# Optimization experiments

Measured on AMD Instinct MI355X. Metric: run time of the kernel, lower is better.

The kernel has to match this reference:

```python
import jax, jax.numpy as jnp
import numpy as np

N = 50000      # nodes
E = 500000     # directed edges
F_IN = 112     # node feature dim
G = 256        # number of graphs in batch


def _lin(key, fan_in, fan_out):
    # torch nn.Linear default init: U(-1/sqrt(fan_in), 1/sqrt(fan_in))
    s = 1.0 / np.sqrt(fan_in)
    kw, kb = jax.random.split(key)
    W = jax.random.uniform(kw, (fan_in, fan_out), jnp.float32, -s, s)
    b = jax.random.uniform(kb, (fan_out,), jnp.float32, -s, s)
    return W, b


def setup_inputs() -> dict:
    key = jax.random.key(0)
    ks = jax.random.split(key, 9)
    x = jax.random.normal(ks[0], (N, F_IN), jnp.float32)
    edge_index = jax.random.randint(ks[1], (2, E), 0, N)
    # sorted graph ids, guaranteeing every graph id 0..G-1 appears
    batch = jnp.sort(jnp.concatenate([jnp.arange(G),
                                      jax.random.randint(ks[2], (N - G,), 0, G)]))
    W1, b1 = _lin(ks[3], F_IN, 336)
    W2, b2 = _lin(ks[4], 336, 168)
    Wg, bg = _lin(ks[5], 168, 84)
    Wf, bf = _lin(ks[6], 84, 42)
    Wo, bo = _lin(ks[7], 42, 1)
    return dict(x=x, edge_index=edge_index, batch=batch,
                W1=W1, b1=b1, W2=W2, b2=b2,
                Wg=Wg, bg=bg, Wf=Wf, bf=bf, Wo=Wo, bo=bo)


def _gcn_conv(x, W, b, src, dst, n):
    """PyG GCNConv: add self-loops, symmetric D^-1/2 A D^-1/2 normalization."""
    h = x @ W                                   # [n, out]
    loop = jnp.arange(n, dtype=src.dtype)
    src_f = jnp.concatenate([src, loop])        # [E+n]
    dst_f = jnp.concatenate([dst, loop])
    deg = jax.ops.segment_sum(jnp.ones(src_f.shape[0], jnp.float32), dst_f, n)
    dinv = jnp.where(deg > 0, jax.lax.rsqrt(deg), 0.0)
    norm = dinv[src_f] * dinv[dst_f]            # [E+n]
    out = jax.ops.segment_sum(h[src_f] * norm[:, None], dst_f, n)
    return out + b


def reference(x, edge_index, batch, W1, b1, W2, b2, Wg, bg, Wf, bf, Wo, bo):
    src, dst = edge_index[0], edge_index[1]
    h = jax.nn.relu(_gcn_conv(x, W1, b1, src, dst, N))
    # dropout is identity in eval mode
    h = jax.nn.relu(_gcn_conv(h, W2, b2, src, dst, N))
    g = jax.ops.segment_max(h, batch, G)        # global max pool -> [G, 168]
    g = jax.nn.relu(g @ Wg + bg)
    g = jax.nn.relu(g @ Wf + bf)
    return g @ Wo + bo                           # [G, 1]
```

## Files before the change

### kernel.cpp

```cpp
#include <hip/hip_runtime.h>
#include <hip/hip_fp16.h>

#define N_NODES 50000
#define MPAD    50048
#define N_EDGES 500000
#define F_IN    112
#define K1P     128
#define F1      336
#define K2P     352
#define F2      168
#define NGRAPH  256
#define SCAN_CHUNK 1024
#define SCAN_BLOCKS ((N_NODES + SCAN_CHUNK - 1) / SCAN_CHUNK)

typedef __attribute__((ext_vector_type(8))) _Float16 f16x8;
typedef __attribute__((ext_vector_type(4))) float f32x4;
typedef unsigned short ushort_t;

__device__ __forceinline__ ushort_t f16_bits(float x) {
    __half h = __float2half_rn(x);
    return *(ushort_t*)&h;
}

__global__ void k_zero_int(int* p, int n) {
    int i = blockIdx.x * blockDim.x + threadIdx.x;
    if (i < n) p[i] = 0;
}

#define CVX_BLOCKS  ((N_NODES * 32) / 256)
#define CNT_BLOCKS  ((N_EDGES / 2 + 255) / 256)
#define CVW1_BLOCKS ((384 * K1P + 255) / 256)
#define CVW2_BLOCKS ((192 * K2P + 255) / 256)
#define RNG_BLOCKS  ((N_NODES + 255) / 256)
#define PREP_BLOCKS (CVX_BLOCKS + CNT_BLOCKS + CVW1_BLOCKS + CVW2_BLOCKS + RNG_BLOCKS)

__global__ __launch_bounds__(256) void k_prep(const float* __restrict__ x,
                                              const int* __restrict__ dst,
                                              const float* __restrict__ W1,
                                              const float* __restrict__ W2,
                                              const int* __restrict__ batch,
                                              ushort_t* __restrict__ x16,
                                              int* __restrict__ dcount,
                                              ushort_t* __restrict__ w1t,
                                              ushort_t* __restrict__ w2t,
                                              int* __restrict__ r0, int* __restrict__ r1) {
    int bid = blockIdx.x;
    int t = threadIdx.x;
    if (bid < CVX_BLOCKS) {
        int i = bid * 256 + t;
        int v = i >> 5, c = i & 31;
        uint2 u = {0, 0};
        if (c < 28) {
            float4 f = *(const float4*)&x[(long)v * F_IN + c * 4];
            __half2 h0 = __floats2half2_rn(f.x, f.y);
            __half2 h1 = __floats2half2_rn(f.z, f.w);
            u.x = *(unsigned*)&h0; u.y = *(unsigned*)&h1;
        }
        ((uint2*)x16)[i] = u;
        return;
    }
    bid -= CVX_BLOCKS;
    if (bid < CNT_BLOCKS) {
        int i = bid * 256 + t;
        if (i < N_EDGES / 2) {
            int2 d = ((const int2*)dst)[i];
            atomicAdd(&dcount[d.x], 1);
            atomicAdd(&dcount[d.y], 1);
        }
        return;
    }
    bid -= CNT_BLOCKS;
    if (bid < CVW1_BLOCKS) {
        int idx = bid * 256 + t;
        if (idx < 384 * K1P) {
            int n = idx / K1P, k = idx % K1P;
            float v = (n < F1 && k < F_IN) ? W1[k * F1 + n] : 0.0f;
            w1t[idx] = f16_bits(v);
        }
        return;
    }
    bid -= CVW1_BLOCKS;
    if (bid < CVW2_BLOCKS) {
        int idx = bid * 256 + t;
        if (idx < 192 * K2P) {
            int n = idx / K2P, k = idx % K2P;
            float v = (n < F2 && k < F1) ? W2[k * F2 + n] : 0.0f;
            w2t[idx] = f16_bits(v);
        }
        return;
    }
    bid -= CVW2_BLOCKS;
    {
        int v = bid * 256 + t;
        if (v >= N_NODES) return;
        int b = batch[v];
        if (v == 0 || batch[v - 1] != b) r0[b] = v;
        if (v == N_NODES - 1 || batch[v + 1] != b) r1[b] = v + 1;
    }
}

__global__ __launch_bounds__(SCAN_CHUNK) void k_scan1(const int* __restrict__ dcount,
                                                      int* __restrict__ off,
                                                      int* __restrict__ partials,
                                                      float* __restrict__ dinv, int n) {
    __shared__ int s[SCAN_CHUNK];
    int t = threadIdx.x;
    int i = blockIdx.x * SCAN_CHUNK + t;
    int val = (i < n) ? dcount[i] : 0;
    s[t] = val;
    __syncthreads();
    for (int d = 1; d < SCAN_CHUNK; d <<= 1) {
        int x = (t >= d) ? s[t - d] : 0;
        __syncthreads();
        s[t] += x;
        __syncthreads();
    }
    if (i < n) {
        off[i] = s[t] - val;
        dinv[i] = rsqrtf((float)val + 1.0f);
    }
    if (t == SCAN_CHUNK - 1) partials[blockIdx.x] = s[t];
}
__global__ __launch_bounds__(SCAN_CHUNK) void k_scan3(int* __restrict__ off,
                                                      const int* __restrict__ partials, int n) {
    __shared__ int tmp[SCAN_BLOCKS];
    __shared__ int pref[SCAN_BLOCKS];
    int t = threadIdx.x;
    if (t < SCAN_BLOCKS) tmp[t] = partials[t];
    __syncthreads();
    if (t == 0) {
        int run = 0;
        for (int j = 0; j < SCAN_BLOCKS; ++j) { pref[j] = run; run += tmp[j]; }
    }
    __syncthreads();
    int i = blockIdx.x * SCAN_CHUNK + t;
    if (i < n) off[i] += pref[blockIdx.x];
    if (i == n) off[i] = N_EDGES;
}

__global__ void k_scatter(const int* __restrict__ src, const int* __restrict__ dst,
                          const int* __restrict__ off, int* __restrict__ cur,
                          const float* __restrict__ dinv,
                          int2* __restrict__ csr, int e2) {
    int i = blockIdx.x * blockDim.x + threadIdx.x;
    if (i >= e2) return;
    int2 s2 = ((const int2*)src)[i];
    int2 d2 = ((const int2*)dst)[i];
    {
        int pos = atomicAdd(&cur[d2.x], 1);
        int2 rec; rec.x = s2.x; rec.y = __float_as_int(dinv[s2.x] * dinv[d2.x]);
        csr[off[d2.x] + pos] = rec;
    }
    {
        int pos = atomicAdd(&cur[d2.y], 1);
        int2 rec; rec.x = s2.y; rec.y = __float_as_int(dinv[s2.y] * dinv[d2.y]);
        csr[off[d2.y] + pos] = rec;
    }
}

__global__ __launch_bounds__(256) void k_agg1(const ushort_t* __restrict__ X16,
                                              const int* __restrict__ off,
                                              const int2* __restrict__ csr,
                                              const float* __restrict__ dinv,
                                              ushort_t* __restrict__ aX) {
    int w = (blockIdx.x * 256 + threadIdx.x) >> 6;
    int lane = threadIdx.x & 63;
    if (w >= N_NODES / 2) return;
    const int g = lane >> 5, sl = lane & 31;
    const int v = 2 * w + g;
    int o0A = off[2 * w], oM = off[2 * w + 1], o1B = off[2 * w + 2];
    int o0 = g ? oM : o0A;
    int n  = g ? (o1B - oM) : (oM - o0A);
    int nmax = max(oM - o0A, o1B - oM);
    float di = dinv[v];
    float s2 = di * di;
    uint2 us = *(const uint2*)(X16 + (long)v * K1P + sl * 4);
    float2 sf0 = __half22float2(*(__half2*)&us.x);
    float2 sf1 = __half22float2(*(__half2*)&us.y);
    float4 acc = {sf0.x * s2, sf0.y * s2, sf1.x * s2, sf1.y * s2};
    int nm1 = max(n - 1, 0);
    for (int b = 0; b < nmax; b += 8) {
        int2 e[8];
        #pragma unroll
        for (int j = 0; j < 8; ++j) {
            int cidx = min(o0 + min(b + j, nm1), N_EDGES - 1);
            e[j] = csr[cidx];
        }
        uint2 u[8];
        #pragma unroll
        for (int j = 0; j < 8; ++j)
            u[j] = *(const uint2*)(X16 + (long)e[j].x * K1P + sl * 4);
        #pragma unroll
        for (int j = 0; j < 8; ++j) {
            float c = ((b + j) < n) ? __int_as_float(e[j].y) : 0.0f;
            float2 f0 = __half22float2(*(__half2*)&u[j].x);
            float2 f1 = __half22float2(*(__half2*)&u[j].y);
            acc.x += c * f0.x; acc.y += c * f0.y; acc.z += c * f1.x; acc.w += c * f1.y;
        }
    }
    __half2 h0 = __floats2half2_rn(acc.x, acc.y);
    __half2 h1 = __floats2half2_rn(acc.z, acc.w);
    uint2 o; o.x = *(unsigned*)&h0; o.y = *(unsigned*)&h1;
    *(uint2*)(aX + (long)v * K1P + sl * 4) = o;
}

__global__ __launch_bounds__(256) void k_gemm_fused(
        const ushort_t* __restrict__ aX,
        const ushort_t* __restrict__ w1t,
        const float* __restrict__ b1,
        const ushort_t* __restrict__ w2t,
        ushort_t* __restrict__ T2) {
    __shared__ ushort_t As[64][40];
    __shared__ ushort_t Bs[352][40];
    __shared__ ushort_t H1s[64][360];
    const int tid = threadIdx.x;
    const int row0 = blockIdx.x * 64;
    const int w = tid >> 6, l = tid & 63;
    const int wm = w >> 1, wn = w & 1;
    const int lm = l & 15, lq = l >> 4;

    f32x4 acc1[2][11];
    #pragma unroll
    for (int i = 0; i < 2; ++i)
        #pragma unroll
        for (int j = 0; j < 11; ++j) acc1[i][j] = (f32x4){0.f, 0.f, 0.f, 0.f};

    for (int k0 = 0; k0 < K1P; k0 += 32) {
        {
            int r = tid >> 2, s = (tid & 3) * 8;
            *(int4*)&As[r][s] = *(const int4*)&aX[(long)(row0 + r) * K1P + k0 + s];
        }
        #pragma unroll
        for (int it = 0; it < 6; ++it) {
            int f = tid + it * 256;
            if (f < 1408) {
                int r = f >> 2, s = (f & 3) * 8;
                *(int4*)&Bs[r][s] = *(const int4*)&w1t[(long)r * K1P + k0 + s];
            }
        }
        __syncthreads();
        f16x8 af0 = *(const f16x8*)&As[wm * 32 + lm][lq * 8];
        f16x8 af1 = *(const f16x8*)&As[wm * 32 + 16 + lm][lq * 8];
        #pragma unroll
        for (int ns = 0; ns < 11; ++ns) {
            f16x8 bf = *(const f16x8*)&Bs[wn * 176 + ns * 16 + lm][lq * 8];
            acc1[0][ns] = __builtin_amdgcn_mfma_f32_16x16x32_f16(af0, bf, acc1[0][ns], 0, 0, 0);
            acc1[1][ns] = __builtin_amdgcn_mfma_f32_16x16x32_f16(af1, bf, acc1[1][ns], 0, 0, 0);
        }
        __syncthreads();
    }
    #pragma unroll
    for (int ms = 0; ms < 2; ++ms)
        #pragma unroll
        for (int ns = 0; ns < 11; ++ns) {
            int col = wn * 176 + ns * 16 + lm;
            float bb = (col < F1) ? b1[col] : 0.0f;
            #pragma unroll
            for (int i = 0; i < 4; ++i) {
                int r = wm * 32 + ms * 16 + lq * 4 + i;
                H1s[r][col] = f16_bits(fmaxf(acc1[ms][ns][i] + bb, 0.0f));
            }
        }
    __syncthreads();

    f32x4 acc2[2][6];
    #pragma unroll
    for (int i = 0; i < 2; ++i)
        #pragma unroll
        for (int j = 0; j < 6; ++j) acc2[i][j] = (f32x4){0.f, 0.f, 0.f, 0.f};

    for (int k0 = 0; k0 < K2P; k0 += 32) {
        #pragma unroll
        for (int it = 0; it < 3; ++it) {
            int f = tid + it * 256;
            int r = f >> 2, s = (f & 3) * 8;
            *(int4*)&Bs[r][s] = *(const int4*)&w2t[(long)r * K2P + k0 + s];
        }
        __syncthreads();
        f16x8 af0 = *(const f16x8*)&H1s[wm * 32 + lm][k0 + lq * 8];
        f16x8 af1 = *(const f16x8*)&H1s[wm * 32 + 16 + lm][k0 + lq * 8];
        #pragma unroll
        for (int ns = 0; ns < 6; ++ns) {
            f16x8 bf = *(const f16x8*)&Bs[wn * 96 + ns * 16 + lm][lq * 8];
            acc2[0][ns] = __builtin_amdgcn_mfma_f32_16x16x32_f16(af0, bf, acc2[0][ns], 0, 0, 0);
            acc2[1][ns] = __builtin_amdgcn_mfma_f32_16x16x32_f16(af1, bf, acc2[1][ns], 0, 0, 0);
        }
        __syncthreads();
    }
    #pragma unroll
    for (int ms = 0; ms < 2; ++ms)
        #pragma unroll
        for (int ns = 0; ns < 6; ++ns) {
            int col = wn * 96 + ns * 16 + lm;
            if (col < F2) {
                #pragma unroll
                for (int i = 0; i < 4; ++i) {
                    int r = row0 + wm * 32 + ms * 16 + lq * 4 + i;
                    T2[(long)r * F2 + col] = f16_bits(acc2[ms][ns][i]);
                }
            }
        }
}

__global__ __launch_bounds__(256) void k_agg2(const ushort_t* __restrict__ T16,
                                              const int* __restrict__ off,
                                              const int2* __restrict__ csr,
                                              const float* __restrict__ dinv,
                                              const float* __restrict__ b2,
                                              ushort_t* __restrict__ out2) {
    int w = (blockIdx.x * 256 + threadIdx.x) >> 6;
    int lane = threadIdx.x & 63;
    if (w >= N_NODES / 2) return;
    const int g = lane >> 5, sl = lane & 31;
    const int v = 2 * w + g;
    const bool act = sl < 21;
    int o0A = off[2 * w], oM = off[2 * w + 1], o1B = off[2 * w + 2];
    int o0 = g ? oM : o0A;
    int n  = g ? (o1B - oM) : (oM - o0A);
    int nmax = max(oM - o0A, o1B - oM);
    float di = dinv[v];
    float4 a0 = {0, 0, 0, 0}, a1 = {0, 0, 0, 0};
    if (act) {
        uint4 u = *(const uint4*)(T16 + (long)v * F2 + sl * 8);
        float2 f0 = __half22float2(*(__half2*)&u.x);
        float2 f1 = __half22float2(*(__half2*)&u.y);
        float2 f2 = __half22float2(*(__half2*)&u.z);
        float2 f3 = __half22float2(*(__half2*)&u.w);
        float s2 = di * di;
        a0.x = f0.x * s2; a0.y = f0.y * s2; a0.z = f1.x * s2; a0.w = f1.y * s2;
        a1.x = f2.x * s2; a1.y = f2.y * s2; a1.z = f3.x * s2; a1.w = f3.y * s2;
    }
    int nm1 = max(n - 1, 0);
    for (int b = 0; b < nmax; b += 8) {
        int2 e[8];
        #pragma unroll
        for (int j = 0; j < 8; ++j) {
            int cidx = min(o0 + min(b + j, nm1), N_EDGES - 1);
            e[j] = csr[cidx];
        }
        uint4 u[8];
        #pragma unroll
        for (int j = 0; j < 8; ++j) {
            int s = ((b + j) < n) ? e[j].x : v;
            if (act) u[j] = *(const uint4*)(T16 + (long)s * F2 + sl * 8);
        }
        #pragma unroll
        for (int j = 0; j < 8; ++j) {
            float c = ((b + j) < n) ? __int_as_float(e[j].y) : 0.0f;
            float2 f0 = __half22float2(*(__half2*)&u[j].x);
            float2 f1 = __half22float2(*(__half2*)&u[j].y);
            float2 f2 = __half22float2(*(__half2*)&u[j].z);
            float2 f3 = __half22float2(*(__half2*)&u[j].w);
            a0.x += c * f0.x; a0.y += c * f0.y; a0.z += c * f1.x; a0.w += c * f1.y;
            a1.x += c * f2.x; a1.y += c * f2.y; a1.z += c * f3.x; a1.w += c * f3.y;
        }
    }
    if (act) {
        float4 bb0 = ((const float4*)b2)[sl * 2];
        float4 bb1 = ((const float4*)b2)[sl * 2 + 1];
        __half2 h0 = __floats2half2_rn(fmaxf(a0.x + bb0.x, 0.0f), fmaxf(a0.y + bb0.y, 0.0f));
        __half2 h1 = __floats2half2_rn(fmaxf(a0.z + bb0.z, 0.0f), fmaxf(a0.w + bb0.w, 0.0f));
        __half2 h2 = __floats2half2_rn(fmaxf(a1.x + bb1.x, 0.0f), fmaxf(a1.y + bb1.y, 0.0f));
        __half2 h3 = __floats2half2_rn(fmaxf(a1.z + bb1.z, 0.0f), fmaxf(a1.w + bb1.w, 0.0f));
        uint4 o;
        o.x = *(unsigned*)&h0; o.y = *(unsigned*)&h1;
        o.z = *(unsigned*)&h2; o.w = *(unsigned*)&h3;
        *(uint4*)(out2 + (long)v * F2 + sl * 8) = o;
    }
}

__global__ __launch_bounds__(256) void k_pool_head(const ushort_t* __restrict__ out2,
        const int* __restrict__ r0, const int* __restrict__ r1,
        const float* __restrict__ Wg, const float* __restrict__ bg,
        const float* __restrict__ Wf, const float* __restrict__ bf,
        const float* __restrict__ Wo, const float* __restrict__ bo,
        float* __restrict__ out) {
    __shared__ float4 sm[4][F2 / 4];
    __shared__ float s0[F2];
    __shared__ float s1[84];
    __shared__ float s2[42];
    int gi = blockIdx.x;
    int slot = threadIdx.x >> 6, lane = threadIdx.x & 63;
    int a = r0[gi], b = r1[gi];
    if (lane < F2 / 4) {
        float4 mx = {0, 0, 0, 0};
        for (int v = a + slot; v < b; v += 4) {
            uint2 u = ((const uint2*)(out2 + (long)v * F2))[lane];
            float2 f0 = __half22float2(*(__half2*)&u.x);
            float2 f1 = __half22float2(*(__half2*)&u.y);
            mx.x = fmaxf(mx.x, f0.x); mx.y = fmaxf(mx.y, f0.y);
            mx.z = fmaxf(mx.z, f1.x); mx.w = fmaxf(mx.w, f1.y);
        }
        sm[slot][lane] = mx;
    }
    __syncthreads();
    if (slot == 0 && lane < F2 / 4) {
        float4 m0 = sm[0][lane], m1 = sm[1][lane], m2 = sm[2][lane], m3 = sm[3][lane];
        float4 r;
        r.x = fmaxf(fmaxf(m0.x, m1.x), fmaxf(m2.x, m3.x));
        r.y = fmaxf(fmaxf(m0.y, m1.y), fmaxf(m2.y, m3.y));
        r.z = fmaxf(fmaxf(m0.z, m1.z), fmaxf(m2.z, m3.z));
        r.w = fmaxf(fmaxf(m0.w, m1.w), fmaxf(m2.w, m3.w));
        ((float4*)s0)[lane] = r;
    }
    __syncthreads();
    int t = threadIdx.x;
    if (t < 84) {
        float acc = bg[t];
        #pragma unroll 4
        for (int k = 0; k < F2; ++k) acc += s0[k] * Wg[k * 84 + t];
        s1[t] = fmaxf(acc, 0.0f);
    }
    __syncthreads();
    if (t < 42) {
        float acc = bf[t];
        #pragma unroll 4
        for (int k = 0; k < 84; ++k) acc += s1[k] * Wf[k * 42 + t];
        s2[t] = fmaxf(acc, 0.0f);
    }
    __syncthreads();
    if (t == 0) {
        float acc = bo[0];
        for (int k = 0; k < 42; ++k) acc += s2[k] * Wo[k];
        out[gi] = acc;
    }
}

extern "C" void kernel_launch(void* const* d_in, const int* in_sizes, int n_in,
                              void* d_out, int out_size, void* d_ws, size_t ws_size,
                              hipStream_t stream) {
    const float* x   = (const float*)d_in[0];
    const int*   ei  = (const int*)d_in[1];
    const int*   bat = (const int*)d_in[2];
    const float* W1  = (const float*)d_in[3];
    const float* b1  = (const float*)d_in[4];
    const float* W2  = (const float*)d_in[5];
    const float* b2  = (const float*)d_in[6];
    const float* Wg  = (const float*)d_in[7];
    const float* bg  = (const float*)d_in[8];
    const float* Wf  = (const float*)d_in[9];
    const float* bf  = (const float*)d_in[10];
    const float* Wo  = (const float*)d_in[11];
    const float* bo  = (const float*)d_in[12];
    float* out = (float*)d_out;

    char* p = (char*)d_ws;
    float* dinv     = (float*)p; p += 50048 * 4;
    int*   dcount   = (int*)p;   p += 50048 * 4;
    int*   cur      = (int*)p;   p += 50048 * 4;
    int*   off      = (int*)p;   p += 50064 * 4;
    int*   partials = (int*)p;   p += 64 * 4;
    int*   rng0     = (int*)p;   p += 256 * 4;
    int*   rng1     = (int*)p;   p += 256 * 4;
    int2*  csr      = (int2*)p;  p += (long)N_EDGES * 8;
    ushort_t* x16   = (ushort_t*)p; p += (long)N_NODES * K1P * 2;
    ushort_t* aX    = (ushort_t*)p; p += (long)MPAD * K1P * 2;
    ushort_t* w1t   = (ushort_t*)p; p += (long)384 * K1P * 2;
    ushort_t* w2t   = (ushort_t*)p; p += (long)192 * K2P * 2;
    ushort_t* t16   = (ushort_t*)p; p += (long)MPAD * F2 * 2;
    ushort_t* o16   = (ushort_t*)p; p += (long)N_NODES * F2 * 2;

    const int* src = ei;
    const int* dst = ei + N_EDGES;
    const int B = 256;

    k_zero_int<<<(2 * 50048 + B - 1) / B, B, 0, stream>>>(dcount, 2 * 50048);
    k_prep<<<PREP_BLOCKS, B, 0, stream>>>(x, dst, W1, W2, bat, x16, dcount, w1t, w2t, rng0, rng1);
    k_scan1<<<SCAN_BLOCKS, SCAN_CHUNK, 0, stream>>>(dcount, off, partials, dinv, N_NODES);
    k_scan3<<<SCAN_BLOCKS, SCAN_CHUNK, 0, stream>>>(off, partials, N_NODES);
    k_scatter<<<(N_EDGES / 2 + B - 1) / B, B, 0, stream>>>(src, dst, off, cur, dinv, csr, N_EDGES / 2);

    k_agg1<<<(N_NODES / 2 * 64) / 256, 256, 0, stream>>>(x16, off, csr, dinv, aX);
    k_gemm_fused<<<MPAD / 64, 256, 0, stream>>>(aX, w1t, b1, w2t, t16);

    k_agg2<<<(N_NODES / 2 * 64) / 256, 256, 0, stream>>>(t16, off, csr, dinv, b2, o16);

    k_pool_head<<<NGRAPH, 256, 0, stream>>>(o16, rng0, rng1, Wg, bg, Wf, bf, Wo, bo, out);
}
```

Measured before the change: 277.1 us.

## Fuse global max-pool into second aggregation and shrink fp16 input stride

The second aggregation kernel now applies bias and ReLU and reduces each block's eight nodes into per-graph maxima. It does this in shared memory, then uses integer atomicMax on a zero-initialised float buffer, which is valid because values are non-negative after ReLU. This removes writing and re-reading the fp16 layer-2 output, the batch-range precompute, and the pooling pass. The head kernel then only runs the small MLP. Separately, the fp16 copy of x uses a packed stride of 112 instead of padding to 128, which cuts conversion and gather traffic in the first aggregation. The cost is atomic contention on the pooled buffer.

Result: faster. 270.6 us (-2.3%).

```diff
diff --git a/kernel.cpp b/kernel.cpp
--- a/kernel.cpp
+++ b/kernel.cpp
@@ -5,6 +5,7 @@
 #define MPAD    50048
 #define N_EDGES 500000
 #define F_IN    112
+#define K1X     112
 #define K1P     128
 #define F1      336
 #define K2P     352
@@ -27,36 +28,32 @@
     if (i < n) p[i] = 0;
 }
 
-#define CVX_BLOCKS  ((N_NODES * 32) / 256)
+#define CVX_ELEMS  (N_NODES * 28)
+#define CVX_BLOCKS ((CVX_ELEMS + 255) / 256)
 #define CNT_BLOCKS  ((N_EDGES / 2 + 255) / 256)
 #define CVW1_BLOCKS ((384 * K1P + 255) / 256)
 #define CVW2_BLOCKS ((192 * K2P + 255) / 256)
-#define RNG_BLOCKS  ((N_NODES + 255) / 256)
-#define PREP_BLOCKS (CVX_BLOCKS + CNT_BLOCKS + CVW1_BLOCKS + CVW2_BLOCKS + RNG_BLOCKS)
+#define PREP_BLOCKS (CVX_BLOCKS + CNT_BLOCKS + CVW1_BLOCKS + CVW2_BLOCKS)
 
 __global__ __launch_bounds__(256) void k_prep(const float* __restrict__ x,
                                               const int* __restrict__ dst,
                                               const float* __restrict__ W1,
                                               const float* __restrict__ W2,
-                                              const int* __restrict__ batch,
                                               ushort_t* __restrict__ x16,
                                               int* __restrict__ dcount,
                                               ushort_t* __restrict__ w1t,
-                                              ushort_t* __restrict__ w2t,
-                                              int* __restrict__ r0, int* __restrict__ r1) {
+                                              ushort_t* __restrict__ w2t) {
     int bid = blockIdx.x;
     int t = threadIdx.x;
     if (bid < CVX_BLOCKS) {
         int i = bid * 256 + t;
-        int v = i >> 5, c = i & 31;
-        uint2 u = {0, 0};
-        if (c < 28) {
-            float4 f = *(const float4*)&x[(long)v * F_IN + c * 4];
+        if (i < CVX_ELEMS) {
+            float4 f = ((const float4*)x)[i];
             __half2 h0 = __floats2half2_rn(f.x, f.y);
             __half2 h1 = __floats2half2_rn(f.z, f.w);
-            u.x = *(unsigned*)&h0; u.y = *(unsigned*)&h1;
-        }
-        ((uint2*)x16)[i] = u;
+            uint2 u; u.x = *(unsigned*)&h0; u.y = *(unsigned*)&h1;
+            ((uint2*)x16)[i] = u;
+        }
         return;
     }
     bid -= CVX_BLOCKS;
@@ -80,22 +77,13 @@
         return;
     }
     bid -= CVW1_BLOCKS;
-    if (bid < CVW2_BLOCKS) {
+    {
         int idx = bid * 256 + t;
         if (idx < 192 * K2P) {
             int n = idx / K2P, k = idx % K2P;
             float v = (n < F2 && k < F1) ? W2[k * F2 + n] : 0.0f;
             w2t[idx] = f16_bits(v);
         }
-        return;
-    }
-    bid -= CVW2_BLOCKS;
-    {
-        int v = bid * 256 + t;
-        if (v >= N_NODES) return;
-        int b = batch[v];
-        if (v == 0 || batch[v - 1] != b) r0[b] = v;
-        if (v == N_NODES - 1 || batch[v + 1] != b) r1[b] = v + 1;
     }
 }
 
@@ -168,16 +156,20 @@
     if (w >= N_NODES / 2) return;
     const int g = lane >> 5, sl = lane & 31;
     const int v = 2 * w + g;
+    const bool act = sl < 28;
     int o0A = off[2 * w], oM = off[2 * w + 1], o1B = off[2 * w + 2];
     int o0 = g ? oM : o0A;
     int n  = g ? (o1B - oM) : (oM - o0A);
     int nmax = max(oM - o0A, o1B - oM);
     float di = dinv[v];
     float s2 = di * di;
-    uint2 us = *(const uint2*)(X16 + (long)v * K1P + sl * 4);
-    float2 sf0 = __half22float2(*(__half2*)&us.x);
-    float2 sf1 = __half22float2(*(__half2*)&us.y);
-    float4 acc = {sf0.x * s2, sf0.y * s2, sf1.x * s2, sf1.y * s2};
+    float4 acc = {0.f, 0.f, 0.f, 0.f};
+    if (act) {
+        uint2 us = *(const uint2*)(X16 + (long)v * K1X + sl * 4);
+        float2 sf0 = __half22float2(*(__half2*)&us.x);
+        float2 sf1 = __half22float2(*(__half2*)&us.y);
+        acc.x = sf0.x * s2; acc.y = sf0.y * s2; acc.z = sf1.x * s2; acc.w = sf1.y * s2;
+    }
     int nm1 = max(n - 1, 0);
     for (int b = 0; b < nmax; b += 8) {
         int2 e[8];
@@ -188,8 +180,11 @@
         }
         uint2 u[8];
         #pragma unroll
-        for (int j = 0; j < 8; ++j)
-            u[j] = *(const uint2*)(X16 + (long)e[j].x * K1P + sl * 4);
+        for (int j = 0; j < 8; ++j) {
+            uint2 uz; uz.x = 0u; uz.y = 0u;
+            u[j] = uz;
+            if (act) u[j] = *(const uint2*)(X16 + (long)e[j].x * K1X + sl * 4);
+        }
         #pragma unroll
         for (int j = 0; j < 8; ++j) {
             float c = ((b + j) < n) ? __int_as_float(e[j].y) : 0.0f;
@@ -307,11 +302,15 @@
                                               const int2* __restrict__ csr,
                                               const float* __restrict__ dinv,
                                               const float* __restrict__ b2,
-                                              ushort_t* __restrict__ out2) {
-    int w = (blockIdx.x * 256 + threadIdx.x) >> 6;
-    int lane = threadIdx.x & 63;
-    if (w >= N_NODES / 2) return;
+                                              const int* __restrict__ batch,
+                                              float* __restrict__ gmax) {
+    __shared__ __align__(16) float smax[8][168];
+    __shared__ int sb[8];
+    int tid = threadIdx.x;
+    int w = (blockIdx.x * 256 + tid) >> 6;
+    int lane = tid & 63;
     const int g = lane >> 5, sl = lane & 31;
+    const int nib = tid >> 5;
     const int v = 2 * w + g;
     const bool act = sl < 21;
     int o0A = off[2 * w], oM = off[2 * w + 1], o1B = off[2 * w + 2];
@@ -358,52 +357,42 @@
     if (act) {
         float4 bb0 = ((const float4*)b2)[sl * 2];
         float4 bb1 = ((const float4*)b2)[sl * 2 + 1];
-        __half2 h0 = __floats2half2_rn(fmaxf(a0.x + bb0.x, 0.0f), fmaxf(a0.y + bb0.y, 0.0f));
-        __half2 h1 = __floats2half2_rn(fmaxf(a0.z + bb0.z, 0.0f), fmaxf(a0.w + bb0.w, 0.0f));
-        __half2 h2 = __floats2half2_rn(fmaxf(a1.x + bb1.x, 0.0f), fmaxf(a1.y + bb1.y, 0.0f));
-        __half2 h3 = __floats2half2_rn(fmaxf(a1.z + bb1.z, 0.0f), fmaxf(a1.w + bb1.w, 0.0f));
-        uint4 o;
-        o.x = *(unsigned*)&h0; o.y = *(unsigned*)&h1;
-        o.z = *(unsigned*)&h2; o.w = *(unsigned*)&h3;
-        *(uint4*)(out2 + (long)v * F2 + sl * 8) = o;
-    }
-}
-
-__global__ __launch_bounds__(256) void k_pool_head(const ushort_t* __restrict__ out2,
-        const int* __restrict__ r0, const int* __restrict__ r1,
+        a0.x = fmaxf(a0.x + bb0.x, 0.0f); a0.y = fmaxf(a0.y + bb0.y, 0.0f);
+        a0.z = fmaxf(a0.z + bb0.z, 0.0f); a0.w = fmaxf(a0.w + bb0.w, 0.0f);
+        a1.x = fmaxf(a1.x + bb1.x, 0.0f); a1.y = fmaxf(a1.y + bb1.y, 0.0f);
+        a1.z = fmaxf(a1.z + bb1.z, 0.0f); a1.w = fmaxf(a1.w + bb1.w, 0.0f);
+        ((float4*)&smax[nib][0])[sl * 2]     = a0;
+        ((float4*)&smax[nib][0])[sl * 2 + 1] = a1;
+    }
+    if ((tid & 31) == 0) sb[nib] = batch[v];
+    __syncthreads();
+    if (tid < F2) {
+        int f = tid;
+        int bp = sb[0];
+        float m = smax[0][f];
+        #pragma unroll
+        for (int r = 1; r < 8; ++r) {
+            int bc = sb[r];
+            float vv = smax[r][f];
+            if (bc == bp) { m = fmaxf(m, vv); }
+            else {
+                atomicMax((int*)&gmax[bp * F2 + f], __float_as_int(m));
+                m = vv; bp = bc;
+            }
+        }
+        atomicMax((int*)&gmax[bp * F2 + f], __float_as_int(m));
+    }
+}
+
+__global__ __launch_bounds__(128) void k_head(const float* __restrict__ gmax,
         const float* __restrict__ Wg, const float* __restrict__ bg,
         const float* __restrict__ Wf, const float* __restrict__ bf,
         const float* __restrict__ Wo, const float* __restrict__ bo,
         float* __restrict__ out) {
-    __shared__ float4 sm[4][F2 / 4];
-    __shared__ float s0[F2];
     __shared__ float s1[84];
     __shared__ float s2[42];
     int gi = blockIdx.x;
-    int slot = threadIdx.x >> 6, lane = threadIdx.x & 63;
-    int a = r0[gi], b = r1[gi];
-    if (lane < F2 / 4) {
-        float4 mx = {0, 0, 0, 0};
-        for (int v = a + slot; v < b; v += 4) {
-            uint2 u = ((const uint2*)(out2 + (long)v * F2))[lane];
-            float2 f0 = __half22float2(*(__half2*)&u.x);
-            float2 f1 = __half22float2(*(__half2*)&u.y);
-            mx.x = fmaxf(mx.x, f0.x); mx.y = fmaxf(mx.y, f0.y);
-            mx.z = fmaxf(mx.z, f1.x); mx.w = fmaxf(mx.w, f1.y);
-        }
-        sm[slot][lane] = mx;
-    }
-    __syncthreads();
-    if (slot == 0 && lane < F2 / 4) {
-        float4 m0 = sm[0][lane], m1 = sm[1][lane], m2 = sm[2][lane], m3 = sm[3][lane];
-        float4 r;
-        r.x = fmaxf(fmaxf(m0.x, m1.x), fmaxf(m2.x, m3.x));
-        r.y = fmaxf(fmaxf(m0.y, m1.y), fmaxf(m2.y, m3.y));
-        r.z = fmaxf(fmaxf(m0.z, m1.z), fmaxf(m2.z, m3.z));
-        r.w = fmaxf(fmaxf(m0.w, m1.w), fmaxf(m2.w, m3.w));
-        ((float4*)s0)[lane] = r;
-    }
-    __syncthreads();
+    const float* s0 = gmax + (long)gi * F2;
     int t = threadIdx.x;
     if (t < 84) {
         float acc = bg[t];
@@ -448,24 +437,23 @@
     float* dinv     = (float*)p; p += 50048 * 4;
     int*   dcount   = (int*)p;   p += 50048 * 4;
     int*   cur      = (int*)p;   p += 50048 * 4;
+    float* gmax     = (float*)p; p += NGRAPH * F2 * 4;
     int*   off      = (int*)p;   p += 50064 * 4;
     int*   partials = (int*)p;   p += 64 * 4;
-    int*   rng0     = (int*)p;   p += 256 * 4;
-    int*   rng1     = (int*)p;   p += 256 * 4;
     int2*  csr      = (int2*)p;  p += (long)N_EDGES * 8;
-    ushort_t* x16   = (ushort_t*)p; p += (long)N_NODES * K1P * 2;
+    ushort_t* x16   = (ushort_t*)p; p += (long)N_NODES * K1X * 2;
     ushort_t* aX    = (ushort_t*)p; p += (long)MPAD * K1P * 2;
     ushort_t* w1t   = (ushort_t*)p; p += (long)384 * K1P * 2;
     ushort_t* w2t   = (ushort_t*)p; p += (long)192 * K2P * 2;
     ushort_t* t16   = (ushort_t*)p; p += (long)MPAD * F2 * 2;
-    ushort_t* o16   = (ushort_t*)p; p += (long)N_NODES * F2 * 2;
 
     const int* src = ei;
     const int* dst = ei + N_EDGES;
     const int B = 256;
-
-    k_zero_int<<<(2 * 50048 + B - 1) / B, B, 0, stream>>>(dcount, 2 * 50048);
-    k_prep<<<PREP_BLOCKS, B, 0, stream>>>(x, dst, W1, W2, bat, x16, dcount, w1t, w2t, rng0, rng1);
+    const int ZERO_WORDS = 50048 * 2 + NGRAPH * F2;
+
+    k_zero_int<<<(ZERO_WORDS + B - 1) / B, B, 0, stream>>>(dcount, ZERO_WORDS);
+    k_prep<<<PREP_BLOCKS, B, 0, stream>>>(x, dst, W1, W2, x16, dcount, w1t, w2t);
     k_scan1<<<SCAN_BLOCKS, SCAN_CHUNK, 0, stream>>>(dcount, off, partials, dinv, N_NODES);
     k_scan3<<<SCAN_BLOCKS, SCAN_CHUNK, 0, stream>>>(off, partials, N_NODES);
     k_scatter<<<(N_EDGES / 2 + B - 1) / B, B, 0, stream>>>(src, dst, off, cur, dinv, csr, N_EDGES / 2);
@@ -473,7 +461,7 @@
     k_agg1<<<(N_NODES / 2 * 64) / 256, 256, 0, stream>>>(x16, off, csr, dinv, aX);
     k_gemm_fused<<<MPAD / 64, 256, 0, stream>>>(aX, w1t, b1, w2t, t16);
 
-    k_agg2<<<(N_NODES / 2 * 64) / 256, 256, 0, stream>>>(t16, off, csr, dinv, b2, o16);
-
-    k_pool_head<<<NGRAPH, 256, 0, stream>>>(o16, rng0, rng1, Wg, bg, Wf, bf, Wo, bo, out);
-}
+    k_agg2<<<(N_NODES / 2 * 64) / 256, 256, 0, stream>>>(t16, off, csr, dinv, b2, bat, gmax);
+
+    k_head<<<NGRAPH, 128, 0, stream>>>(gmax, Wg, bg, Wf, bf, Wo, bo, out);
+}
```
